# Optimization experiments

Measured on AMD Instinct MI355X. Metric: run time of the kernel, lower is better.

The kernel has to match this reference:

```python
import jax, jax.numpy as jnp
import numpy as np

NUM_HEADS = 16
HEAD_DIM = 64  # hidden_size 1024 / 16 heads


def setup_inputs() -> dict:
    key = jax.random.key(0)
    ks = jax.random.split(key, 4)
    B, S, H = 2, 2048, 1024
    scale = 1.0 / np.sqrt(H)
    return {
        "hidden_states": jax.random.normal(ks[0], (B, S, H), dtype=jnp.float32),
        "attention_mask": jnp.zeros((B, 1, 1, S), dtype=jnp.float32),
        "Wq": jax.random.normal(ks[1], (H, H), dtype=jnp.float32) * scale,
        "bq": jnp.zeros((H,), dtype=jnp.float32),
        "Wk": jax.random.normal(ks[2], (H, H), dtype=jnp.float32) * scale,
        "bk": jnp.zeros((H,), dtype=jnp.float32),
        "Wv": jax.random.normal(ks[3], (H, H), dtype=jnp.float32) * scale,
        "bv": jnp.zeros((H,), dtype=jnp.float32),
    }


def reference(hidden_states, attention_mask, Wq, bq, Wk, bk, Wv, bv):
    B, S, H = hidden_states.shape
    h, d = NUM_HEADS, HEAD_DIM

    def heads(x):  # [B,S,H] -> [B,h,S,d]
        return x.reshape(B, S, h, d).transpose(0, 2, 1, 3)

    q = heads(hidden_states @ Wq + bq)
    k = heads(hidden_states @ Wk + bk)
    v = heads(hidden_states @ Wv + bv)

    # [B,h,S,S] scores, scaled then additive-masked (HF BERT semantics)
    scores = jnp.einsum("bhqd,bhkd->bhqk", q, k) / jnp.sqrt(jnp.float32(d))
    scores = scores + attention_mask
    probs = jax.nn.softmax(scores, axis=-1)  # dropout p=0 -> identity

    ctx = jnp.einsum("bhqk,bhkd->bhqd", probs, v)
    ctx = ctx.transpose(0, 2, 1, 3).reshape(B, S, H)
    return ctx
```

## Files before the change

### kernel.cpp

```cpp
#include <hip/hip_runtime.h>
#include <hip/hip_bf16.h>


#define SEQ   2048
#define HID   1024
#define NHEAD 16
#define HD    64
#define SD    ((size_t)SEQ * HD)

typedef __bf16 bf16x8 __attribute__((ext_vector_type(8)));
typedef float  f32x4  __attribute__((ext_vector_type(4)));

#define L2E 1.4426950408889634f
#define SOFT_OFF 16.0f

__device__ __forceinline__ unsigned short f2b(float f) {
    unsigned int x = __float_as_uint(f);
    x += 0x7FFFu + ((x >> 16) & 1u);
    return (unsigned short)(x >> 16);
}

__global__ __launch_bounds__(256) void cvt_x_k(const float* __restrict__ X,
                                               unsigned short* __restrict__ Xb)
{
    const size_t i = ((size_t)blockIdx.x * 256 + threadIdx.x) * 4;
    const float4 v = *(const float4*)(X + i);
    ushort4 o;
    o.x = f2b(v.x); o.y = f2b(v.y); o.z = f2b(v.z); o.w = f2b(v.w);
    *(ushort4*)(Xb + i) = o;
}

__global__ __launch_bounds__(256) void cvt_w_k(
    const float* __restrict__ Wq, const float* __restrict__ Wk,
    const float* __restrict__ Wv, unsigned short* __restrict__ Wtb)
{
    __shared__ __align__(16) unsigned short T[64][68];
    const int z = blockIdx.z;
    const float* __restrict__ W = (z == 0) ? Wq : (z == 1) ? Wk : Wv;
    const int k0 = blockIdx.x * 64, n0 = blockIdx.y * 64;
    const int tid = threadIdx.x;
    #pragma unroll
    for (int it = 0; it < 16; ++it) {
        const int idx = 256 * it + tid;
        const int r = idx >> 6, c = idx & 63;
        T[c][r] = f2b(W[(size_t)(k0 + r) * HID + n0 + c]);
    }
    __syncthreads();
    unsigned short* dst = Wtb + (size_t)z * HID * HID;
    #pragma unroll
    for (int it = 0; it < 4; ++it) {
        const int idx = 256 * it + tid;
        const int n = idx >> 4, c4 = (idx & 15) * 4;
        *(ushort4*)(dst + (size_t)(n0 + n) * HID + k0 + c4) = *(ushort4*)&T[n][c4];
    }
}

__device__ __forceinline__ void gemm_epilogue(
    f32x4 acc[4][4], const float* __restrict__ Bp,
    unsigned short* __restrict__ scratch, unsigned short (*Et)[68],
    int z, int m0, int n0, int wr, int wc, int ln, int quad)
{
    const int b = m0 >> 11;
    const int srow0 = (m0 + wr) & (SEQ - 1);
    const int head = (n0 + wc) >> 6;
    __syncthreads();

    if (z == 2) {
        #pragma unroll
        for (int half = 0; half < 2; ++half) {
            #pragma unroll
            for (int nt2 = 0; nt2 < 2; ++nt2) {
                const int nt = half * 2 + nt2;
                const float bias = Bp[n0 + wc + nt * 16 + ln];
                #pragma unroll
                for (int mt = 0; mt < 4; ++mt) {
                    ushort4 o;
                    o.x = f2b(acc[mt][nt][0] + bias);
                    o.y = f2b(acc[mt][nt][1] + bias);
                    o.z = f2b(acc[mt][nt][2] + bias);
                    o.w = f2b(acc[mt][nt][3] + bias);
                    *(ushort4*)&Et[nt2 * 16 + ln][mt * 16 + quad * 4] = o;
                }
            }
            __syncthreads();
            #pragma unroll
            for (int it = 0; it < 8; ++it) {
                const int d = it * 4 + quad, s4 = ln * 4;
                *(ushort4*)(scratch +
                    ((size_t)(64 + b * NHEAD + head) * HD + half * 32 + d) * SEQ
                    + srow0 + s4) = *(const ushort4*)&Et[d][s4];
            }
            __syncthreads();
        }
    } else {
        #pragma unroll
        for (int half = 0; half < 2; ++half) {
            #pragma unroll
            for (int mt2 = 0; mt2 < 2; ++mt2) {
                const int mt = half * 2 + mt2;
                #pragma unroll
                for (int nt = 0; nt < 4; ++nt) {
                    const float bias = Bp[n0 + wc + nt * 16 + ln];
                    #pragma unroll
                    for (int r = 0; r < 4; ++r)
                        Et[mt2 * 16 + quad * 4 + r][nt * 16 + ln] =
                            f2b(acc[mt][nt][r] + bias);
                }
            }
            __syncthreads();
            #pragma unroll
            for (int it = 0; it < 8; ++it) {
                const int r = it * 4 + quad, c4 = ln * 4;
                *(ushort4*)(scratch +
                    ((size_t)(z * 32 + b * NHEAD + head) * SEQ + srow0
                     + half * 32 + r) * HD + c4) = *(const ushort4*)&Et[r][c4];
            }
            __syncthreads();
        }
    }
}

__global__ __launch_bounds__(256) void qkv_gemm_bf16(
    const unsigned short* __restrict__ Xb, const unsigned short* __restrict__ Wtb,
    const float* __restrict__ bq, const float* __restrict__ bk,
    const float* __restrict__ bv, unsigned short* __restrict__ scratch)
{
    __shared__ __align__(16) unsigned char pool[20480];
    unsigned short (*Xs)[40] = (unsigned short (*)[40])pool;
    unsigned short (*Wt)[40] = (unsigned short (*)[40])(pool + 10240);

    const int z = blockIdx.z;
    const float* __restrict__ Bp = (z == 0) ? bq : (z == 1) ? bk : bv;
    const unsigned short* __restrict__ Wz = Wtb + (size_t)z * HID * HID;

    const int tid = threadIdx.x, w = tid >> 6, lane = tid & 63;
    const int ln = lane & 15, quad = lane >> 4;
    const int wr = (w >> 1) * 64, wc = (w & 1) * 64;
    const int m0 = blockIdx.x * 128, n0 = blockIdx.y * 128;
    const int sr = tid >> 2, c8 = (tid & 3) * 8;

    f32x4 acc[4][4];
    #pragma unroll
    for (int i = 0; i < 4; ++i)
        #pragma unroll
        for (int j = 0; j < 4; ++j) acc[i][j] = (f32x4){0.f, 0.f, 0.f, 0.f};

    uint4 xg0 = *(const uint4*)(Xb + (size_t)(m0 + sr) * HID + c8);
    uint4 xg1 = *(const uint4*)(Xb + (size_t)(m0 + sr + 64) * HID + c8);
    uint4 wg0 = *(const uint4*)(Wz + (size_t)(n0 + sr) * HID + c8);
    uint4 wg1 = *(const uint4*)(Wz + (size_t)(n0 + sr + 64) * HID + c8);

    for (int k0 = 0; k0 < HID; k0 += 32) {
        __syncthreads();
        *(uint4*)&Xs[sr][c8]      = xg0;
        *(uint4*)&Xs[sr + 64][c8] = xg1;
        *(uint4*)&Wt[sr][c8]      = wg0;
        *(uint4*)&Wt[sr + 64][c8] = wg1;
        __syncthreads();
        const int kn = (k0 + 32) & (HID - 1);
        xg0 = *(const uint4*)(Xb + (size_t)(m0 + sr) * HID + kn + c8);
        xg1 = *(const uint4*)(Xb + (size_t)(m0 + sr + 64) * HID + kn + c8);
        wg0 = *(const uint4*)(Wz + (size_t)(n0 + sr) * HID + kn + c8);
        wg1 = *(const uint4*)(Wz + (size_t)(n0 + sr + 64) * HID + kn + c8);

        bf16x8 am[4], bn[4];
        #pragma unroll
        for (int t = 0; t < 4; ++t) {
            am[t] = *(const bf16x8*)&Xs[wr + t * 16 + ln][quad * 8];
            bn[t] = *(const bf16x8*)&Wt[wc + t * 16 + ln][quad * 8];
        }
        #pragma unroll
        for (int mt = 0; mt < 4; ++mt)
            #pragma unroll
            for (int nt = 0; nt < 4; ++nt)
                acc[mt][nt] = __builtin_amdgcn_mfma_f32_16x16x32_bf16(
                    am[mt], bn[nt], acc[mt][nt], 0, 0, 0);
    }
    unsigned short (*Et)[68] = (unsigned short (*)[68])(pool + (size_t)w * 4352);
    gemm_epilogue(acc, Bp, scratch, Et, z, m0, n0, wr, wc, ln, quad);
}

__global__ __launch_bounds__(256) void qkv_gemm_fp32(
    const float* __restrict__ X,
    const float* __restrict__ Wq, const float* __restrict__ bq,
    const float* __restrict__ Wk, const float* __restrict__ bk,
    const float* __restrict__ Wv, const float* __restrict__ bv,
    unsigned short* __restrict__ scratch)
{
    __shared__ __align__(16) unsigned char pool[20480];
    unsigned short (*Xs)[40] = (unsigned short (*)[40])pool;
    unsigned short (*Wt)[40] = (unsigned short (*)[40])(pool + 10240);

    const int z = blockIdx.z;
    const float* __restrict__ W  = (z == 0) ? Wq : (z == 1) ? Wk : Wv;
    const float* __restrict__ Bp = (z == 0) ? bq : (z == 1) ? bk : bv;

    const int tid = threadIdx.x, w = tid >> 6, lane = tid & 63;
    const int ln = lane & 15, quad = lane >> 4;
    const int wr = (w >> 1) * 64, wc = (w & 1) * 64;
    const int m0 = blockIdx.x * 128, n0 = blockIdx.y * 128;

    const int xr = tid >> 3, xc = (tid & 7) * 4;
    const int wkr = tid >> 5, wnc = (tid & 31) * 4;

    f32x4 acc[4][4];
    #pragma unroll
    for (int i = 0; i < 4; ++i)
        #pragma unroll
        for (int j = 0; j < 4; ++j) acc[i][j] = (f32x4){0.f, 0.f, 0.f, 0.f};

    for (int k0 = 0; k0 < HID; k0 += 32) {
        __syncthreads();
        #pragma unroll
        for (int it = 0; it < 4; ++it) {
            const int r = xr + 32 * it;
            const float4 xv = *(const float4*)(X + (size_t)(m0 + r) * HID + k0 + xc);
            ushort4 xb;
            xb.x = f2b(xv.x); xb.y = f2b(xv.y); xb.z = f2b(xv.z); xb.w = f2b(xv.w);
            *(ushort4*)&Xs[r][xc] = xb;
            const int kr = wkr + 8 * it;
            const float4 wv = *(const float4*)(W + (size_t)(k0 + kr) * HID + n0 + wnc);
            Wt[wnc + 0][kr] = f2b(wv.x);
            Wt[wnc + 1][kr] = f2b(wv.y);
            Wt[wnc + 2][kr] = f2b(wv.z);
            Wt[wnc + 3][kr] = f2b(wv.w);
        }
        __syncthreads();
        bf16x8 am[4], bn[4];
        #pragma unroll
        for (int t = 0; t < 4; ++t) {
            am[t] = *(const bf16x8*)&Xs[wr + t * 16 + ln][quad * 8];
            bn[t] = *(const bf16x8*)&Wt[wc + t * 16 + ln][quad * 8];
        }
        #pragma unroll
        for (int mt = 0; mt < 4; ++mt)
            #pragma unroll
            for (int nt = 0; nt < 4; ++nt)
                acc[mt][nt] = __builtin_amdgcn_mfma_f32_16x16x32_bf16(
                    am[mt], bn[nt], acc[mt][nt], 0, 0, 0);
    }
    unsigned short (*Et)[68] = (unsigned short (*)[68])(pool + (size_t)w * 4352);
    gemm_epilogue(acc, Bp, scratch, Et, z, m0, n0, wr, wc, ln, quad);
}

__global__ __launch_bounds__(256) void attn_mfma(
    const unsigned short* __restrict__ scratch,
    const float* __restrict__ mask,
    float* __restrict__ out)
{
    __shared__ __align__(16) unsigned char smem[27648];
    unsigned short (*Ks)[72] = (unsigned short (*)[72])smem;
    unsigned short (*Vt)[72] = (unsigned short (*)[72])(smem + 9216);
    unsigned short (*Ps)[72] = (unsigned short (*)[72])(smem + 18432);
    float (*Obuf)[68] = (float (*)[68])smem;

    const int qt = blockIdx.x;
    const int bh = blockIdx.y;
    const int b = bh >> 4, head = bh & 15;

    const unsigned short* __restrict__ Qp  = scratch + (size_t)bh * SD;
    const unsigned short* __restrict__ Kp  = scratch + (size_t)(32 + bh) * SD;
    const unsigned short* __restrict__ Vtp = scratch + (size_t)(64 + bh) * SD;
    const float* __restrict__ maskp = mask + b * SEQ;

    const int tid = threadIdx.x, w = tid >> 6, lane = tid & 63;
    const int ln = lane & 15, quad = lane >> 4;

    const int qrow = qt * 64 + w * 16 + ln;
    const bf16x8 qb0 = *(const bf16x8*)(Qp + (size_t)qrow * HD + quad * 8);
    const bf16x8 qb1 = *(const bf16x8*)(Qp + (size_t)qrow * HD + 32 + quad * 8);

    f32x4 O[4];
    #pragma unroll
    for (int t = 0; t < 4; ++t) O[t] = (f32x4){0.f, 0.f, 0.f, 0.f};
    float lr = 0.0f;

    const int sr8 = tid >> 3, sc8 = (tid & 7) * 8;

    uint4 kg0 = *(const uint4*)(Kp + (size_t)sr8 * HD + sc8);
    uint4 kg1 = *(const uint4*)(Kp + (size_t)(sr8 + 32) * HD + sc8);
    uint4 vg0 = *(const uint4*)(Vtp + (size_t)sr8 * SEQ + sc8);
    uint4 vg1 = *(const uint4*)(Vtp + (size_t)(sr8 + 32) * SEQ + sc8);

    for (int kt = 0; kt < 32; ++kt) {
        __syncthreads();
        *(uint4*)&Ks[sr8][sc8]      = kg0;
        *(uint4*)&Ks[sr8 + 32][sc8] = kg1;
        *(uint4*)&Vt[sr8][sc8]      = vg0;
        *(uint4*)&Vt[sr8 + 32][sc8] = vg1;
        __syncthreads();
        const int kn = (kt + 1) & 31;
        kg0 = *(const uint4*)(Kp + (size_t)(kn * 64 + sr8) * HD + sc8);
        kg1 = *(const uint4*)(Kp + (size_t)(kn * 64 + sr8 + 32) * HD + sc8);
        vg0 = *(const uint4*)(Vtp + (size_t)sr8 * SEQ + kn * 64 + sc8);
        vg1 = *(const uint4*)(Vtp + (size_t)(sr8 + 32) * SEQ + kn * 64 + sc8);

        f32x4 s[4];
        #pragma unroll
        for (int t = 0; t < 4; ++t) {
            const bf16x8 ka0 = *(const bf16x8*)&Ks[t * 16 + ln][quad * 8];
            const bf16x8 ka1 = *(const bf16x8*)&Ks[t * 16 + ln][32 + quad * 8];
            f32x4 a = (f32x4){0.f, 0.f, 0.f, 0.f};
            a = __builtin_amdgcn_mfma_f32_16x16x32_bf16(ka0, qb0, a, 0, 0, 0);
            a = __builtin_amdgcn_mfma_f32_16x16x32_bf16(ka1, qb1, a, 0, 0, 0);
            s[t] = a;
        }

        const float c = 0.125f * L2E;
        #pragma unroll
        for (int t = 0; t < 4; ++t) {
            const float4 mk4 = *(const float4*)(maskp + kt * 64 + t * 16 + quad * 4);
            const float b0 = fmaf(mk4.x, L2E, -SOFT_OFF);
            const float b1 = fmaf(mk4.y, L2E, -SOFT_OFF);
            const float b2 = fmaf(mk4.z, L2E, -SOFT_OFF);
            const float b3 = fmaf(mk4.w, L2E, -SOFT_OFF);
            const float p0 = exp2f(fmaf(s[t][0], c, b0));
            const float p1 = exp2f(fmaf(s[t][1], c, b1));
            const float p2 = exp2f(fmaf(s[t][2], c, b2));
            const float p3 = exp2f(fmaf(s[t][3], c, b3));
            lr += (p0 + p1) + (p2 + p3);
            unsigned int w0, w1;
            asm("v_cvt_pk_bf16_f32 %0, %1, %2" : "=v"(w0) : "v"(p0), "v"(p1));
            asm("v_cvt_pk_bf16_f32 %0, %1, %2" : "=v"(w1) : "v"(p2), "v"(p3));
            uint2 pw; pw.x = w0; pw.y = w1;
            *(uint2*)&Ps[w * 16 + ln][t * 16 + quad * 4] = pw;
        }

        const bf16x8 pb0 = *(const bf16x8*)&Ps[w * 16 + ln][quad * 8];
        const bf16x8 pb1 = *(const bf16x8*)&Ps[w * 16 + ln][32 + quad * 8];
        #pragma unroll
        for (int t = 0; t < 4; ++t) {
            const bf16x8 va0 = *(const bf16x8*)&Vt[t * 16 + ln][quad * 8];
            const bf16x8 va1 = *(const bf16x8*)&Vt[t * 16 + ln][32 + quad * 8];
            O[t] = __builtin_amdgcn_mfma_f32_16x16x32_bf16(va0, pb0, O[t], 0, 0, 0);
            O[t] = __builtin_amdgcn_mfma_f32_16x16x32_bf16(va1, pb1, O[t], 0, 0, 0);
        }
    }

    lr += __shfl_xor(lr, 16);
    lr += __shfl_xor(lr, 32);

    __syncthreads();
    const float inv = 1.0f / lr;
    #pragma unroll
    for (int t = 0; t < 4; ++t) {
        float4 o4;
        o4.x = O[t][0] * inv; o4.y = O[t][1] * inv;
        o4.z = O[t][2] * inv; o4.w = O[t][3] * inv;
        *(float4*)&Obuf[w * 16 + ln][t * 16 + quad * 4] = o4;
    }
    __syncthreads();
    #pragma unroll
    for (int it = 0; it < 4; ++it) {
        const int r = (tid >> 4) + 16 * it, c4 = (tid & 15) * 4;
        *(float4*)(out + ((size_t)b * SEQ + qt * 64 + r) * HID + head * HD + c4)
            = *(const float4*)&Obuf[r][c4];
    }
}

extern "C" void kernel_launch(void* const* d_in, const int* in_sizes, int n_in,
                              void* d_out, int out_size, void* d_ws, size_t ws_size,
                              hipStream_t stream) {
    const float* X    = (const float*)d_in[0];
    const float* mask = (const float*)d_in[1];
    const float* Wq   = (const float*)d_in[2];
    const float* bq   = (const float*)d_in[3];
    const float* Wk   = (const float*)d_in[4];
    const float* bk   = (const float*)d_in[5];
    const float* Wv   = (const float*)d_in[6];
    const float* bv   = (const float*)d_in[7];

    unsigned short* scratch = (unsigned short*)d_ws;
    float* out = (float*)d_out;

    const bool big = (ws_size >= (40ull << 20));
    if (big) {
        unsigned short* Xb  = scratch + 96 * SD;
        unsigned short* Wtb = Xb + (size_t)2 * SEQ * HID;
        cvt_x_k<<<4096, 256, 0, stream>>>(X, Xb);
        cvt_w_k<<<dim3(16, 16, 3), 256, 0, stream>>>(Wq, Wk, Wv, Wtb);
        qkv_gemm_bf16<<<dim3(32, 8, 3), 256, 0, stream>>>(
            Xb, Wtb, bq, bk, bv, scratch);
    } else {
        qkv_gemm_fp32<<<dim3(32, 8, 3), 256, 0, stream>>>(
            X, Wq, bq, Wk, bk, Wv, bv, scratch);
    }
    attn_mfma<<<dim3(SEQ / 64, 32), 256, 0, stream>>>(scratch, mask, out);
}
```

Baseline: 216.7 us.

## Widen attention query tile to 128 rows and deepen GEMM k-tile to 64

The attention kernel now runs 512 threads per block covering 128 query rows. Each K/V tile staged in LDS is shared by eight waves instead of four, which halves global K/V traffic per query row and the number of staging loads per thread. The bf16 QKV GEMM stages a 64-wide k-slice per iteration instead of 32, halving the number of barriers, and adds a 3-blocks-per-CU occupancy hint. The cost is more LDS per block and fewer attention blocks (512), which may reduce latency hiding and occupancy.

```diff
diff --git a/kernel.cpp b/kernel.cpp
--- a/kernel.cpp
+++ b/kernel.cpp
@@ -120,14 +120,14 @@
     }
 }
 
-__global__ __launch_bounds__(256) void qkv_gemm_bf16(
+__global__ __launch_bounds__(256, 3) void qkv_gemm_bf16(
     const unsigned short* __restrict__ Xb, const unsigned short* __restrict__ Wtb,
     const float* __restrict__ bq, const float* __restrict__ bk,
     const float* __restrict__ bv, unsigned short* __restrict__ scratch)
 {
-    __shared__ __align__(16) unsigned char pool[20480];
-    unsigned short (*Xs)[40] = (unsigned short (*)[40])pool;
-    unsigned short (*Wt)[40] = (unsigned short (*)[40])(pool + 10240);
+    __shared__ __align__(16) unsigned char pool[36864];
+    unsigned short (*Xs)[72] = (unsigned short (*)[72])pool;
+    unsigned short (*Wt)[72] = (unsigned short (*)[72])(pool + 18432);
 
     const int z = blockIdx.z;
     const float* __restrict__ Bp = (z == 0) ? bq : (z == 1) ? bk : bv;
@@ -137,7 +137,7 @@
     const int ln = lane & 15, quad = lane >> 4;
     const int wr = (w >> 1) * 64, wc = (w & 1) * 64;
     const int m0 = blockIdx.x * 128, n0 = blockIdx.y * 128;
-    const int sr = tid >> 2, c8 = (tid & 3) * 8;
+    const int sr = tid >> 3, c8 = (tid & 7) * 8;
 
     f32x4 acc[4][4];
     #pragma unroll
@@ -145,36 +145,43 @@
         #pragma unroll
         for (int j = 0; j < 4; ++j) acc[i][j] = (f32x4){0.f, 0.f, 0.f, 0.f};
 
-    uint4 xg0 = *(const uint4*)(Xb + (size_t)(m0 + sr) * HID + c8);
-    uint4 xg1 = *(const uint4*)(Xb + (size_t)(m0 + sr + 64) * HID + c8);
-    uint4 wg0 = *(const uint4*)(Wz + (size_t)(n0 + sr) * HID + c8);
-    uint4 wg1 = *(const uint4*)(Wz + (size_t)(n0 + sr + 64) * HID + c8);
-
-    for (int k0 = 0; k0 < HID; k0 += 32) {
-        __syncthreads();
-        *(uint4*)&Xs[sr][c8]      = xg0;
-        *(uint4*)&Xs[sr + 64][c8] = xg1;
-        *(uint4*)&Wt[sr][c8]      = wg0;
-        *(uint4*)&Wt[sr + 64][c8] = wg1;
-        __syncthreads();
-        const int kn = (k0 + 32) & (HID - 1);
-        xg0 = *(const uint4*)(Xb + (size_t)(m0 + sr) * HID + kn + c8);
-        xg1 = *(const uint4*)(Xb + (size_t)(m0 + sr + 64) * HID + kn + c8);
-        wg0 = *(const uint4*)(Wz + (size_t)(n0 + sr) * HID + kn + c8);
-        wg1 = *(const uint4*)(Wz + (size_t)(n0 + sr + 64) * HID + kn + c8);
-
-        bf16x8 am[4], bn[4];
-        #pragma unroll
-        for (int t = 0; t < 4; ++t) {
-            am[t] = *(const bf16x8*)&Xs[wr + t * 16 + ln][quad * 8];
-            bn[t] = *(const bf16x8*)&Wt[wc + t * 16 + ln][quad * 8];
-        }
-        #pragma unroll
-        for (int mt = 0; mt < 4; ++mt)
-            #pragma unroll
-            for (int nt = 0; nt < 4; ++nt)
-                acc[mt][nt] = __builtin_amdgcn_mfma_f32_16x16x32_bf16(
-                    am[mt], bn[nt], acc[mt][nt], 0, 0, 0);
+    uint4 xg[4], wg[4];
+    #pragma unroll
+    for (int it = 0; it < 4; ++it) {
+        xg[it] = *(const uint4*)(Xb + (size_t)(m0 + sr + 32 * it) * HID + c8);
+        wg[it] = *(const uint4*)(Wz + (size_t)(n0 + sr + 32 * it) * HID + c8);
+    }
+
+    for (int k0 = 0; k0 < HID; k0 += 64) {
+        __syncthreads();
+        #pragma unroll
+        for (int it = 0; it < 4; ++it) {
+            *(uint4*)&Xs[sr + 32 * it][c8] = xg[it];
+            *(uint4*)&Wt[sr + 32 * it][c8] = wg[it];
+        }
+        __syncthreads();
+        const int kn = (k0 + 64) & (HID - 1);
+        #pragma unroll
+        for (int it = 0; it < 4; ++it) {
+            xg[it] = *(const uint4*)(Xb + (size_t)(m0 + sr + 32 * it) * HID + kn + c8);
+            wg[it] = *(const uint4*)(Wz + (size_t)(n0 + sr + 32 * it) * HID + kn + c8);
+        }
+
+        #pragma unroll
+        for (int kk = 0; kk < 2; ++kk) {
+            bf16x8 am[4], bn[4];
+            #pragma unroll
+            for (int t = 0; t < 4; ++t) {
+                am[t] = *(const bf16x8*)&Xs[wr + t * 16 + ln][kk * 32 + quad * 8];
+                bn[t] = *(const bf16x8*)&Wt[wc + t * 16 + ln][kk * 32 + quad * 8];
+            }
+            #pragma unroll
+            for (int mt = 0; mt < 4; ++mt)
+                #pragma unroll
+                for (int nt = 0; nt < 4; ++nt)
+                    acc[mt][nt] = __builtin_amdgcn_mfma_f32_16x16x32_bf16(
+                        am[mt], bn[nt], acc[mt][nt], 0, 0, 0);
+        }
     }
     unsigned short (*Et)[68] = (unsigned short (*)[68])(pool + (size_t)w * 4352);
     gemm_epilogue(acc, Bp, scratch, Et, z, m0, n0, wr, wc, ln, quad);
@@ -243,12 +250,12 @@
     gemm_epilogue(acc, Bp, scratch, Et, z, m0, n0, wr, wc, ln, quad);
 }
 
-__global__ __launch_bounds__(256) void attn_mfma(
+__global__ __launch_bounds__(512) void attn_mfma(
     const unsigned short* __restrict__ scratch,
     const float* __restrict__ mask,
     float* __restrict__ out)
 {
-    __shared__ __align__(16) unsigned char smem[27648];
+    __shared__ __align__(16) unsigned char smem[36864];
     unsigned short (*Ks)[72] = (unsigned short (*)[72])smem;
     unsigned short (*Vt)[72] = (unsigned short (*)[72])(smem + 9216);
     unsigned short (*Ps)[72] = (unsigned short (*)[72])(smem + 18432);
@@ -266,7 +273,7 @@
     const int tid = threadIdx.x, w = tid >> 6, lane = tid & 63;
     const int ln = lane & 15, quad = lane >> 4;
 
-    const int qrow = qt * 64 + w * 16 + ln;
+    const int qrow = qt * 128 + w * 16 + ln;
     const bf16x8 qb0 = *(const bf16x8*)(Qp + (size_t)qrow * HD + quad * 8);
     const bf16x8 qb1 = *(const bf16x8*)(Qp + (size_t)qrow * HD + 32 + quad * 8);
 
@@ -277,23 +284,17 @@
 
     const int sr8 = tid >> 3, sc8 = (tid & 7) * 8;
 
-    uint4 kg0 = *(const uint4*)(Kp + (size_t)sr8 * HD + sc8);
-    uint4 kg1 = *(const uint4*)(Kp + (size_t)(sr8 + 32) * HD + sc8);
-    uint4 vg0 = *(const uint4*)(Vtp + (size_t)sr8 * SEQ + sc8);
-    uint4 vg1 = *(const uint4*)(Vtp + (size_t)(sr8 + 32) * SEQ + sc8);
+    uint4 kg = *(const uint4*)(Kp + (size_t)sr8 * HD + sc8);
+    uint4 vg = *(const uint4*)(Vtp + (size_t)sr8 * SEQ + sc8);
 
     for (int kt = 0; kt < 32; ++kt) {
         __syncthreads();
-        *(uint4*)&Ks[sr8][sc8]      = kg0;
-        *(uint4*)&Ks[sr8 + 32][sc8] = kg1;
-        *(uint4*)&Vt[sr8][sc8]      = vg0;
-        *(uint4*)&Vt[sr8 + 32][sc8] = vg1;
+        *(uint4*)&Ks[sr8][sc8] = kg;
+        *(uint4*)&Vt[sr8][sc8] = vg;
         __syncthreads();
         const int kn = (kt + 1) & 31;
-        kg0 = *(const uint4*)(Kp + (size_t)(kn * 64 + sr8) * HD + sc8);
-        kg1 = *(const uint4*)(Kp + (size_t)(kn * 64 + sr8 + 32) * HD + sc8);
-        vg0 = *(const uint4*)(Vtp + (size_t)sr8 * SEQ + kn * 64 + sc8);
-        vg1 = *(const uint4*)(Vtp + (size_t)(sr8 + 32) * SEQ + kn * 64 + sc8);
+        kg = *(const uint4*)(Kp + (size_t)(kn * 64 + sr8) * HD + sc8);
+        vg = *(const uint4*)(Vtp + (size_t)sr8 * SEQ + kn * 64 + sc8);
 
         f32x4 s[4];
         #pragma unroll
@@ -352,8 +353,8 @@
     __syncthreads();
     #pragma unroll
     for (int it = 0; it < 4; ++it) {
-        const int r = (tid >> 4) + 16 * it, c4 = (tid & 15) * 4;
-        *(float4*)(out + ((size_t)b * SEQ + qt * 64 + r) * HID + head * HD + c4)
+        const int r = (tid >> 4) + 32 * it, c4 = (tid & 15) * 4;
+        *(float4*)(out + ((size_t)b * SEQ + qt * 128 + r) * HID + head * HD + c4)
             = *(const float4*)&Obuf[r][c4];
     }
 }
@@ -385,5 +386,5 @@
         qkv_gemm_fp32<<<dim3(32, 8, 3), 256, 0, stream>>>(
             X, Wq, bq, Wk, bk, Wv, bv, scratch);
     }
-    attn_mfma<<<dim3(SEQ / 64, 32), 256, 0, stream>>>(scratch, mask, out);
-}
+    attn_mfma<<<dim3(SEQ / 128, 32), 512, 0, stream>>>(scratch, mask, out);
+}
```

Result: slower. 279.4 us (+28.9%).

## Double-buffer K/V tiles in attention and remap blocks for XCD locality

Applied to the files above, without the earlier changes.

The attention kernel now keeps two LDS buffers for K and V and prefetches two tiles ahead, which removes one of the two barriers per iteration. The grid becomes 1D and the block index is remapped so that blocks of the same head land on the same XCD, so K/V reuse in L2 should improve. The cost is larger LDS use (about 45KB per block), which may lower occupancy.

```diff
diff --git a/kernel.cpp b/kernel.cpp
--- a/kernel.cpp
+++ b/kernel.cpp
@@ -248,14 +248,16 @@
     const float* __restrict__ mask,
     float* __restrict__ out)
 {
-    __shared__ __align__(16) unsigned char smem[27648];
-    unsigned short (*Ks)[72] = (unsigned short (*)[72])smem;
-    unsigned short (*Vt)[72] = (unsigned short (*)[72])(smem + 9216);
-    unsigned short (*Ps)[72] = (unsigned short (*)[72])(smem + 18432);
+    __shared__ __align__(16) unsigned char smem[46080];
+    unsigned short (*Ks)[64][72] = (unsigned short (*)[64][72])smem;
+    unsigned short (*Vt)[64][72] = (unsigned short (*)[64][72])(smem + 18432);
+    unsigned short (*Ps)[72]     = (unsigned short (*)[72])(smem + 36864);
     float (*Obuf)[68] = (float (*)[68])smem;
 
-    const int qt = blockIdx.x;
-    const int bh = blockIdx.y;
+    const int orig = blockIdx.x;
+    const int wg = ((orig & 7) << 7) + (orig >> 3);
+    const int qt = wg & 31;
+    const int bh = wg >> 5;
     const int b = bh >> 4, head = bh & 15;
 
     const unsigned short* __restrict__ Qp  = scratch + (size_t)bh * SD;
@@ -277,29 +279,43 @@
 
     const int sr8 = tid >> 3, sc8 = (tid & 7) * 8;
 
-    uint4 kg0 = *(const uint4*)(Kp + (size_t)sr8 * HD + sc8);
-    uint4 kg1 = *(const uint4*)(Kp + (size_t)(sr8 + 32) * HD + sc8);
-    uint4 vg0 = *(const uint4*)(Vtp + (size_t)sr8 * SEQ + sc8);
-    uint4 vg1 = *(const uint4*)(Vtp + (size_t)(sr8 + 32) * SEQ + sc8);
+    {
+        uint4 a = *(const uint4*)(Kp + (size_t)sr8 * HD + sc8);
+        uint4 c = *(const uint4*)(Kp + (size_t)(sr8 + 32) * HD + sc8);
+        uint4 d = *(const uint4*)(Vtp + (size_t)sr8 * SEQ + sc8);
+        uint4 e = *(const uint4*)(Vtp + (size_t)(sr8 + 32) * SEQ + sc8);
+        *(uint4*)&Ks[0][sr8][sc8]      = a;
+        *(uint4*)&Ks[0][sr8 + 32][sc8] = c;
+        *(uint4*)&Vt[0][sr8][sc8]      = d;
+        *(uint4*)&Vt[0][sr8 + 32][sc8] = e;
+    }
+    uint4 kg0 = *(const uint4*)(Kp + (size_t)(64 + sr8) * HD + sc8);
+    uint4 kg1 = *(const uint4*)(Kp + (size_t)(64 + sr8 + 32) * HD + sc8);
+    uint4 vg0 = *(const uint4*)(Vtp + (size_t)sr8 * SEQ + 64 + sc8);
+    uint4 vg1 = *(const uint4*)(Vtp + (size_t)(sr8 + 32) * SEQ + 64 + sc8);
+    __syncthreads();
 
     for (int kt = 0; kt < 32; ++kt) {
-        __syncthreads();
-        *(uint4*)&Ks[sr8][sc8]      = kg0;
-        *(uint4*)&Ks[sr8 + 32][sc8] = kg1;
-        *(uint4*)&Vt[sr8][sc8]      = vg0;
-        *(uint4*)&Vt[sr8 + 32][sc8] = vg1;
-        __syncthreads();
-        const int kn = (kt + 1) & 31;
-        kg0 = *(const uint4*)(Kp + (size_t)(kn * 64 + sr8) * HD + sc8);
-        kg1 = *(const uint4*)(Kp + (size_t)(kn * 64 + sr8 + 32) * HD + sc8);
-        vg0 = *(const uint4*)(Vtp + (size_t)sr8 * SEQ + kn * 64 + sc8);
-        vg1 = *(const uint4*)(Vtp + (size_t)(sr8 + 32) * SEQ + kn * 64 + sc8);
+        const int cur = kt & 1;
+        if (kt < 31) {
+            *(uint4*)&Ks[cur ^ 1][sr8][sc8]      = kg0;
+            *(uint4*)&Ks[cur ^ 1][sr8 + 32][sc8] = kg1;
+            *(uint4*)&Vt[cur ^ 1][sr8][sc8]      = vg0;
+            *(uint4*)&Vt[cur ^ 1][sr8 + 32][sc8] = vg1;
+        }
+        if (kt < 30) {
+            const int kn = kt + 2;
+            kg0 = *(const uint4*)(Kp + (size_t)(kn * 64 + sr8) * HD + sc8);
+            kg1 = *(const uint4*)(Kp + (size_t)(kn * 64 + sr8 + 32) * HD + sc8);
+            vg0 = *(const uint4*)(Vtp + (size_t)sr8 * SEQ + kn * 64 + sc8);
+            vg1 = *(const uint4*)(Vtp + (size_t)(sr8 + 32) * SEQ + kn * 64 + sc8);
+        }
 
         f32x4 s[4];
         #pragma unroll
         for (int t = 0; t < 4; ++t) {
-            const bf16x8 ka0 = *(const bf16x8*)&Ks[t * 16 + ln][quad * 8];
-            const bf16x8 ka1 = *(const bf16x8*)&Ks[t * 16 + ln][32 + quad * 8];
+            const bf16x8 ka0 = *(const bf16x8*)&Ks[cur][t * 16 + ln][quad * 8];
+            const bf16x8 ka1 = *(const bf16x8*)&Ks[cur][t * 16 + ln][32 + quad * 8];
             f32x4 a = (f32x4){0.f, 0.f, 0.f, 0.f};
             a = __builtin_amdgcn_mfma_f32_16x16x32_bf16(ka0, qb0, a, 0, 0, 0);
             a = __builtin_amdgcn_mfma_f32_16x16x32_bf16(ka1, qb1, a, 0, 0, 0);
@@ -330,17 +346,18 @@
         const bf16x8 pb1 = *(const bf16x8*)&Ps[w * 16 + ln][32 + quad * 8];
         #pragma unroll
         for (int t = 0; t < 4; ++t) {
-            const bf16x8 va0 = *(const bf16x8*)&Vt[t * 16 + ln][quad * 8];
-            const bf16x8 va1 = *(const bf16x8*)&Vt[t * 16 + ln][32 + quad * 8];
+            const bf16x8 va0 = *(const bf16x8*)&Vt[cur][t * 16 + ln][quad * 8];
+            const bf16x8 va1 = *(const bf16x8*)&Vt[cur][t * 16 + ln][32 + quad * 8];
             O[t] = __builtin_amdgcn_mfma_f32_16x16x32_bf16(va0, pb0, O[t], 0, 0, 0);
             O[t] = __builtin_amdgcn_mfma_f32_16x16x32_bf16(va1, pb1, O[t], 0, 0, 0);
         }
+
+        __syncthreads();
     }
 
     lr += __shfl_xor(lr, 16);
     lr += __shfl_xor(lr, 32);
 
-    __syncthreads();
     const float inv = 1.0f / lr;
     #pragma unroll
     for (int t = 0; t < 4; ++t) {
@@ -385,5 +402,5 @@
         qkv_gemm_fp32<<<dim3(32, 8, 3), 256, 0, stream>>>(
             X, Wq, bq, Wk, bk, Wv, bv, scratch);
     }
-    attn_mfma<<<dim3(SEQ / 64, 32), 256, 0, stream>>>(scratch, mask, out);
-}
+    attn_mfma<<<1024, 256, 0, stream>>>(scratch, mask, out);
+}
```

Result: no change. 214.8 us (-0.9%).
